# Kernel optimization log

Measured on AMD Instinct MI355X. Metric: run time of the kernel, lower is better.

The kernel has to match this reference:

```python
import jax, jax.numpy as jnp
import numpy as np

EPS = 1e-6
B, S, H, I = 4, 2048, 2048, 8192  # batch, seq, hidden(embed), intermediate(mlp)
N_ACT = 2  # gated: ('gelu', 'linear')


def setup_inputs() -> dict:
    key = jax.random.key(0)
    k_x, k_k1, k_k2 = jax.random.split(key, 3)
    x = jax.random.normal(k_x, (B, S, H), dtype=jnp.float32)
    scale = jnp.ones((H,), dtype=jnp.float32)          # layernorm gamma (ones init)
    ln_bias = jnp.zeros((H,), dtype=jnp.float32)       # layernorm beta (zeros init)
    # kernel_1: (hidden, n_activations, intermediate); kernel_2: (intermediate, hidden)
    kernel_1 = jax.random.normal(k_k1, (H, N_ACT, I), dtype=jnp.float32) * 0.02
    kernel_2 = jax.random.normal(k_k2, (I, H), dtype=jnp.float32) * 0.02
    return {"x": x, "scale": scale, "ln_bias": ln_bias, "kernel_1": kernel_1, "kernel_2": kernel_2}


def reference(x, scale, ln_bias, kernel_1, kernel_2):
    # LayerNorm over last axis (zero_centered_gamma=False)
    mean = jnp.mean(x, axis=-1, keepdims=True)
    var = jnp.mean(jnp.square(x - mean), axis=-1, keepdims=True)
    ln = (x - mean) * jax.lax.rsqrt(var + EPS) * scale + ln_bias  # [B,S,H]
    # Dense 1: project to (n_activations, intermediate)
    y = jnp.einsum('bsh,hai->bsai', ln, kernel_1)  # [B,S,2,I]
    # Gated activation: gelu(y0) * linear(y1)  (flax nn.gelu default approximate=True)
    z = jax.nn.gelu(y[..., 0, :], approximate=True) * y[..., 1, :]  # [B,S,I]
    # Dense 2: project back to hidden
    out = jnp.einsum('bsi,ih->bsh', z, kernel_2)  # [B,S,H]
    return out
```

## Files before the change

### kernel.cpp

```cpp
#include <hip/hip_runtime.h>
#include <hip/hip_bf16.h>

#define DEVINL __device__ __forceinline__

typedef __attribute__((ext_vector_type(8))) __bf16 bf16x8;
typedef __attribute__((ext_vector_type(4))) float f32x4;
typedef __attribute__((ext_vector_type(4))) unsigned short us4;

DEVINL unsigned short f2bf(float f) {
  union { float f; unsigned int u; } c;
  c.f = f;
  unsigned int u = c.u;
  u += 0x7fffu + ((u >> 16) & 1u);
  return (unsigned short)(u >> 16);
}

DEVINL float gelu_tanh(float x) {
  float t = 1.5957691216057308f * x * __builtin_fmaf(0.044715f, x * x, 1.0f);
  return x / (1.0f + __expf(-t));
}

DEVINL void ld16(const void* g, void* l) {
  __builtin_amdgcn_global_load_lds(
      (const __attribute__((address_space(1))) void*)g,
      (__attribute__((address_space(3))) void*)l, 16, 0, 0);
}

__global__ __launch_bounds__(256) void transpose_cast_kernel(
    const float* __restrict__ in, unsigned short* __restrict__ out, int R, int C) {
  __shared__ float tile[32][33];
  const int t = threadIdx.x;
  const int r0 = blockIdx.x << 5, c0 = blockIdx.y << 5;
  const int tr = t >> 3, tc = (t & 7) << 2;
  const float4 v = *(const float4*)(in + (size_t)(r0 + tr) * C + c0 + tc);
  tile[tr][tc] = v.x; tile[tr][tc + 1] = v.y;
  tile[tr][tc + 2] = v.z; tile[tr][tc + 3] = v.w;
  __syncthreads();
  us4 o;
  o[0] = f2bf(tile[tc + 0][tr]);
  o[1] = f2bf(tile[tc + 1][tr]);
  o[2] = f2bf(tile[tc + 2][tr]);
  o[3] = f2bf(tile[tc + 3][tr]);
  *(us4*)(out + (size_t)(c0 + tr) * R + r0 + tc) = o;
}

__global__ __launch_bounds__(256) void ln_kernel(
    const float* __restrict__ x, const float* __restrict__ gamma,
    const float* __restrict__ beta, unsigned short* __restrict__ out) {
  constexpr int H = 2048;
  const int t = threadIdx.x;
  const size_t row = blockIdx.x;
  const float4* xr = (const float4*)(x + row * H);
  const float4 a = xr[t], b = xr[t + 256];
  float s  = a.x + a.y + a.z + a.w + b.x + b.y + b.z + b.w;
  float s2 = a.x*a.x + a.y*a.y + a.z*a.z + a.w*a.w
           + b.x*b.x + b.y*b.y + b.z*b.z + b.w*b.w;
#pragma unroll
  for (int o = 32; o > 0; o >>= 1) { s += __shfl_xor(s, o); s2 += __shfl_xor(s2, o); }
  __shared__ float red[8];
  const int wid = t >> 6, lane = t & 63;
  if (lane == 0) { red[wid] = s; red[4 + wid] = s2; }
  __syncthreads();
  s  = red[0] + red[1] + red[2] + red[3];
  s2 = red[4] + red[5] + red[6] + red[7];
  const float mean = s * (1.0f / H);
  const float rstd = rsqrtf(s2 * (1.0f / H) - mean * mean + 1e-6f);
  const float4 g0 = ((const float4*)gamma)[t], g1 = ((const float4*)gamma)[t + 256];
  const float4 c0 = ((const float4*)beta)[t],  c1 = ((const float4*)beta)[t + 256];
  us4 o0, o1;
  o0[0] = f2bf((a.x - mean) * rstd * g0.x + c0.x);
  o0[1] = f2bf((a.y - mean) * rstd * g0.y + c0.y);
  o0[2] = f2bf((a.z - mean) * rstd * g0.z + c0.z);
  o0[3] = f2bf((a.w - mean) * rstd * g0.w + c0.w);
  o1[0] = f2bf((b.x - mean) * rstd * g1.x + c1.x);
  o1[1] = f2bf((b.y - mean) * rstd * g1.y + c1.y);
  o1[2] = f2bf((b.z - mean) * rstd * g1.z + c1.z);
  o1[3] = f2bf((b.w - mean) * rstd * g1.w + c1.w);
  *(us4*)(out + row * H + (size_t)t * 4) = o0;
  *(us4*)(out + row * H + 1024 + (size_t)t * 4) = o1;
}

template<int KDIM, bool GATED>
__global__ __launch_bounds__(512, 2) void gemm8p(
    const unsigned short* __restrict__ Amat,
    const unsigned short* __restrict__ Bm0,
    const unsigned short* __restrict__ Bm1,
    void* __restrict__ outp, int mCount) {
  constexpr int NT = KDIM / 64;
  __shared__ char lds[131072];
  const int t = threadIdx.x, lane = t & 63, wid = t >> 6;
  const int wr = wid >> 2, wc = wid & 3;
  const int bid = (int)blockIdx.x;
  int mb, nb;
  if (GATED && mCount >= 8) {
    const int xcd = bid & 7, l = bid >> 3;
    const int g = l >> 5, l32 = l & 31;
    const int mchunks = mCount >> 3;
    const int quad = g / mchunks, mch = g % mchunks;
    mb = (mch << 3) | (l32 & 7);
    nb = (xcd << 3) | (quad << 2) | (l32 >> 3);
  } else {
    const int nwg = (int)gridDim.x, q = nwg >> 3;
    const int wg = (bid & 7) * q + (bid >> 3);
    mb = wg % mCount; nb = wg / mCount;
  }
  const size_t m0 = (size_t)mb << 8;
  const size_t nrow = (size_t)nb * (GATED ? 128 : 256);
  const unsigned short* aSrc  = Amat + m0 * KDIM;
  const unsigned short* b0Src = Bm0 + nrow * KDIM;
  const unsigned short* b1Src = Bm1 + nrow * KDIM;

  const int srow = (wid << 3) + (lane >> 3);
  const int sOff = srow * KDIM + (((lane & 7) ^ (srow & 7)) << 3);

  const int fr = lane & 15, l16 = lane >> 4;
  const int c0 = (l16 ^ (fr & 7)) << 4;
  const int c1 = ((4 | l16) ^ (fr & 7)) << 4;
  const int aRowOff = ((wr << 6) + fr) << 7;
  const int bRowOff = ((wc << 5) + fr) << 7;

  f32x4 acc[2][2][4][2] = {};

  auto stageU = [&](const unsigned short* src, int ldsOff, int k0) {
    const unsigned short* s = src + sOff + k0;
    ld16(s, lds + ldsOff + (wid << 10));
    ld16(s + (size_t)64 * KDIM, lds + ldsOff + 8192 + (wid << 10));
  };

#define READ_A(dst_, ab_)                                                     \
  _Pragma("unroll") for (int m = 0; m < 4; ++m) {                             \
    dst_[0][m] = *(const bf16x8*)((ab_) + aRowOff + m * 2048 + c0);           \
    dst_[1][m] = *(const bf16x8*)((ab_) + aRowOff + m * 2048 + c1);           \
  }
#define READ_B(dst_, bb_)                                                     \
  _Pragma("unroll") for (int n = 0; n < 2; ++n) {                             \
    dst_[0][n] = *(const bf16x8*)((bb_) + bRowOff + n * 2048 + c0);           \
    dst_[1][n] = *(const bf16x8*)((bb_) + bRowOff + n * 2048 + c1);           \
  }
#define MFMA16(mh_, g_, bsrc_)                                                \
  __builtin_amdgcn_s_setprio(1);                                              \
  _Pragma("unroll") for (int m = 0; m < 4; ++m)                               \
    _Pragma("unroll") for (int n = 0; n < 2; ++n) {                           \
      acc[mh_][g_][m][n] = __builtin_amdgcn_mfma_f32_16x16x32_bf16(           \
          af[0][m], bsrc_[0][n], acc[mh_][g_][m][n], 0, 0, 0);                \
      acc[mh_][g_][m][n] = __builtin_amdgcn_mfma_f32_16x16x32_bf16(           \
          af[1][m], bsrc_[1][n], acc[mh_][g_][m][n], 0, 0, 0);                \
    }                                                                         \
  __builtin_amdgcn_s_setprio(0);
#define LGKM(n_)                                                              \
  asm volatile("s_waitcnt lgkmcnt(" #n_ ")" ::: "memory");                    \
  __builtin_amdgcn_sched_barrier(0);

  stageU(aSrc, 0, 0);
  stageU(b0Src, 32768, 0);
  stageU(aSrc + (size_t)128 * KDIM, 16384, 0);
  stageU(b1Src, 49152, 0);
  stageU(aSrc, 65536, 64);
  stageU(b0Src, 65536 + 32768, 64);
  asm volatile("s_waitcnt vmcnt(4)" ::: "memory");
  __builtin_amdgcn_s_barrier();

  for (int tt = 0; tt < NT; ++tt) {
    const int c = tt & 1, cn = c ^ 1;
    const int t1 = (tt + 1 < NT) ? tt + 1 : NT - 1;
    const int t2 = (tt + 2 < NT) ? tt + 2 : NT - 1;
    const int k1b = t1 << 6, k2b = t2 << 6;
    const int cb = c << 16, cnb = cn << 16;
    const char* base = lds + cb;
    bf16x8 af[2][4], b0r[2][2], b1r[2][2];

    READ_A(af, base);
    READ_B(b0r, base + 32768);
    READ_B(b1r, base + 49152);
    stageU(aSrc + (size_t)128 * KDIM, cnb + 16384, k1b);
    LGKM(4);
    MFMA16(0, 0, b0r);
    LGKM(0);
    MFMA16(0, 1, b1r);
    READ_A(af, base + 16384);
    stageU(b1Src, cnb + 49152, k1b);
    __builtin_amdgcn_s_barrier();
    LGKM(0);
    MFMA16(1, 1, b1r);
    MFMA16(1, 0, b0r);
    stageU(aSrc, cb, k2b);
    stageU(b0Src, cb + 32768, k2b);
    asm volatile("s_waitcnt vmcnt(4)" ::: "memory");
    __builtin_amdgcn_s_barrier();
  }
  asm volatile("s_waitcnt vmcnt(0)" ::: "memory");
#undef READ_A
#undef READ_B
#undef MFMA16
#undef LGKM

  const int fq = (lane >> 4) << 2;
  if constexpr (GATED) {
    unsigned short* Z = (unsigned short*)outp;
#pragma unroll
    for (int mh = 0; mh < 2; ++mh)
#pragma unroll
      for (int m = 0; m < 4; ++m)
#pragma unroll
        for (int n = 0; n < 2; ++n) {
          const size_t row = m0 + (mh << 7) + (wr << 6) + (m << 4) + fq;
          const size_t col = ((size_t)nb << 7) + (wc << 5) + (n << 4) + fr;
#pragma unroll
          for (int rr = 0; rr < 4; ++rr) {
            const float y0 = acc[mh][0][m][n][rr];
            const float y1 = acc[mh][1][m][n][rr];
            Z[(row + rr) * 8192 + col] = f2bf(gelu_tanh(y0) * y1);
          }
        }
  } else {
    float* O = (float*)outp;
#pragma unroll
    for (int mh = 0; mh < 2; ++mh)
#pragma unroll
      for (int g = 0; g < 2; ++g)
#pragma unroll
        for (int m = 0; m < 4; ++m)
#pragma unroll
          for (int n = 0; n < 2; ++n) {
            const size_t row = m0 + (mh << 7) + (wr << 6) + (m << 4) + fq;
            const size_t col = ((size_t)nb << 8) + (g << 7) + (wc << 5) + (n << 4) + fr;
#pragma unroll
            for (int rr = 0; rr < 4; ++rr)
              O[(row + rr) * 2048 + col] = acc[mh][g][m][n][rr];
          }
  }
}

extern "C" void kernel_launch(void* const* d_in, const int* in_sizes, int n_in,
                              void* d_out, int out_size, void* d_ws, size_t ws_size,
                              hipStream_t stream) {
  const float* x     = (const float*)d_in[0];
  const float* gamma = (const float*)d_in[1];
  const float* beta  = (const float*)d_in[2];
  const float* k1    = (const float*)d_in[3];
  const float* k2    = (const float*)d_in[4];
  float* out = (float*)d_out;

  const size_t H = 2048, I = 8192, M = 8192;
  unsigned short* k1T = (unsigned short*)d_ws;
  unsigned short* k2T = k1T + 2 * I * H;
  unsigned short* lnb = k2T + H * I;
  unsigned short* zb  = lnb + M * H;

  const size_t fixedB = (2 * I * H + H * I + M * H) * 2;
  int nc = 1;
  while (nc < 32 && fixedB + (M / nc) * I * 2 > ws_size) nc <<= 1;

  transpose_cast_kernel<<<dim3(H / 32, (2 * I) / 32), 256, 0, stream>>>(
      k1, k1T, (int)H, (int)(2 * I));
  transpose_cast_kernel<<<dim3(I / 32, H / 32), 256, 0, stream>>>(
      k2, k2T, (int)I, (int)H);
  ln_kernel<<<dim3((unsigned)M), 256, 0, stream>>>(x, gamma, beta, lnb);

  const size_t Mc = M / nc;
  const int mC = (int)(Mc / 256);
  for (int c = 0; c < nc; ++c) {
    gemm8p<2048, true><<<dim3((unsigned)(mC * 64)), 512, 0, stream>>>(
        lnb + c * Mc * H, k1T, k1T + (size_t)8192 * 2048, zb, mC);
    gemm8p<8192, false><<<dim3((unsigned)(mC * 8)), 512, 0, stream>>>(
        zb, k2T, k2T + (size_t)128 * 8192, out + c * Mc * H, mC);
  }
}
```

Measured before the change: 770.5 us.

## Software-pipeline LDS fragment reads across K tiles with double register sets

Restructures the GEMM main loop so the next tile's LDS fragment reads are issued before the second half of the current tile's MFMAs, using two alternating register sets (X/Y) and a loop unrolled by two. Global staging loads are also moved earlier in each tile. The aim is to hide LDS read latency behind MFMA work instead of stalling at the start of each iteration. In exchange it raises register pressure, which could lower occupancy or cause spills, and it assumes NT is even.

```diff
diff --git a/kernel.cpp b/kernel.cpp
--- a/kernel.cpp
+++ b/kernel.cpp
@@ -137,19 +137,20 @@
     dst_[0][n] = *(const bf16x8*)((bb_) + bRowOff + n * 2048 + c0);           \
     dst_[1][n] = *(const bf16x8*)((bb_) + bRowOff + n * 2048 + c1);           \
   }
-#define MFMA16(mh_, g_, bsrc_)                                                \
+#define MFMA16(mh_, g_, afr_, bsrc_)                                          \
   __builtin_amdgcn_s_setprio(1);                                              \
   _Pragma("unroll") for (int m = 0; m < 4; ++m)                               \
     _Pragma("unroll") for (int n = 0; n < 2; ++n) {                           \
       acc[mh_][g_][m][n] = __builtin_amdgcn_mfma_f32_16x16x32_bf16(           \
-          af[0][m], bsrc_[0][n], acc[mh_][g_][m][n], 0, 0, 0);                \
+          afr_[0][m], bsrc_[0][n], acc[mh_][g_][m][n], 0, 0, 0);              \
       acc[mh_][g_][m][n] = __builtin_amdgcn_mfma_f32_16x16x32_bf16(           \
-          af[1][m], bsrc_[1][n], acc[mh_][g_][m][n], 0, 0, 0);                \
+          afr_[1][m], bsrc_[1][n], acc[mh_][g_][m][n], 0, 0, 0);              \
     }                                                                         \
   __builtin_amdgcn_s_setprio(0);
 #define LGKM(n_)                                                              \
   asm volatile("s_waitcnt lgkmcnt(" #n_ ")" ::: "memory");                    \
   __builtin_amdgcn_sched_barrier(0);
+#define SCHED0 __builtin_amdgcn_sched_barrier(0)
 
   stageU(aSrc, 0, 0);
   stageU(b0Src, 32768, 0);
@@ -160,39 +161,53 @@
   asm volatile("s_waitcnt vmcnt(4)" ::: "memory");
   __builtin_amdgcn_s_barrier();
 
-  for (int tt = 0; tt < NT; ++tt) {
-    const int c = tt & 1, cn = c ^ 1;
-    const int t1 = (tt + 1 < NT) ? tt + 1 : NT - 1;
-    const int t2 = (tt + 2 < NT) ? tt + 2 : NT - 1;
-    const int k1b = t1 << 6, k2b = t2 << 6;
-    const int cb = c << 16, cnb = cn << 16;
-    const char* base = lds + cb;
-    bf16x8 af[2][4], b0r[2][2], b1r[2][2];
-
-    READ_A(af, base);
-    READ_B(b0r, base + 32768);
-    READ_B(b1r, base + 49152);
-    stageU(aSrc + (size_t)128 * KDIM, cnb + 16384, k1b);
-    LGKM(4);
-    MFMA16(0, 0, b0r);
-    LGKM(0);
-    MFMA16(0, 1, b1r);
-    READ_A(af, base + 16384);
-    stageU(b1Src, cnb + 49152, k1b);
-    __builtin_amdgcn_s_barrier();
-    LGKM(0);
-    MFMA16(1, 1, b1r);
-    MFMA16(1, 0, b0r);
-    stageU(aSrc, cb, k2b);
-    stageU(b0Src, cb + 32768, k2b);
-    asm volatile("s_waitcnt vmcnt(4)" ::: "memory");
-    __builtin_amdgcn_s_barrier();
-  }
-  asm volatile("s_waitcnt vmcnt(0)" ::: "memory");
+  bf16x8 afX[2][4], b0X[2][2], b1X[2][2];
+  bf16x8 afY[2][4], b0Y[2][2], b1Y[2][2];
+  READ_A(afX, lds);          SCHED0;
+  READ_B(b0X, lds + 32768);  SCHED0;
+  READ_B(b1X, lds + 49152);  SCHED0;
+
+#define TILE(tt_, cb_, cnb_, AF, B0R, B1R, AFN, B0N, B1N)                      \
+  {                                                                            \
+    const int t1 = ((tt_) + 1 < NT) ? (tt_) + 1 : NT - 1;                      \
+    const int t2 = ((tt_) + 2 < NT) ? (tt_) + 2 : NT - 1;                      \
+    const int k1b = t1 << 6, k2b = t2 << 6;                                    \
+    const char* base = lds + (cb_);                                            \
+    const char* nbase = lds + (cnb_);                                          \
+                                                                       \
+    LGKM(4);                                            \
+    stageU(aSrc + (size_t)128 * KDIM, (cnb_) + 16384, k1b);     \
+    stageU(b1Src, (cnb_) + 49152, k1b);                         \
+    MFMA16(0, 0, AF, B0R);                                                     \
+    LGKM(0);                                                    \
+    MFMA16(0, 1, AF, B1R);                                                     \
+    READ_A(AF, base + 16384); SCHED0;               \
+    __builtin_amdgcn_s_barrier();                                   \
+    LGKM(0);                                                  \
+                                                                       \
+    stageU(aSrc, (cb_), k2b);                                   \
+    stageU(b0Src, (cb_) + 32768, k2b);                          \
+    asm volatile("s_waitcnt vmcnt(4)" ::: "memory");     \
+    SCHED0;                                                                    \
+    __builtin_amdgcn_s_barrier();                                   \
+    READ_A(AFN, nbase);           SCHED0;           \
+    READ_B(B0N, nbase + 32768);   SCHED0;                                      \
+    READ_B(B1N, nbase + 49152);   SCHED0;                                      \
+    MFMA16(1, 1, AF, B1R);                        \
+    MFMA16(1, 0, AF, B0R);                                                     \
+  }
+
+  for (int tt = 0; tt < NT; tt += 2) {
+    TILE(tt,     0,     65536, afX, b0X, b1X, afY, b0Y, b1Y);
+    TILE(tt + 1, 65536, 0,     afY, b0Y, b1Y, afX, b0X, b1X);
+  }
+  asm volatile("s_waitcnt vmcnt(0) lgkmcnt(0)" ::: "memory");
+#undef TILE
 #undef READ_A
 #undef READ_B
 #undef MFMA16
 #undef LGKM
+#undef SCHED0
 
   const int fq = (lane >> 4) << 2;
   if constexpr (GATED) {
```

After: 2.567 ms. +233.1%, slower.

## Load B operand directly from global into registers, deepen A LDS ring to four slots

Applied to the files above, without the earlier changes.

The B (weight) operand is no longer staged through LDS; each wave loads its B fragments straight from global memory into double-buffered registers one tile ahead. LDS now holds only the A tile, arranged as a four-slot ring with a two-tile prefetch distance, and the main loop is unrolled by four to rotate slots and register buffers. The aim is to cut LDS traffic and ds_read work for B and spend LDS on deeper A prefetch. In exchange, B global loads are not shared across the waves that need the same columns, which raises global/L2 traffic and register pressure, and latency hiding now depends on the vmcnt waits.

```diff
diff --git a/kernel.cpp b/kernel.cpp
--- a/kernel.cpp
+++ b/kernel.cpp
@@ -81,7 +81,7 @@
 }
 
 template<int KDIM, bool GATED>
-__global__ __launch_bounds__(512, 2) void gemm8p(
+__global__ __launch_bounds__(512, 2) void gemm_bd(
     const unsigned short* __restrict__ Amat,
     const unsigned short* __restrict__ Bm0,
     const unsigned short* __restrict__ Bm1,
@@ -117,82 +117,89 @@
   const int c0 = (l16 ^ (fr & 7)) << 4;
   const int c1 = ((4 | l16) ^ (fr & 7)) << 4;
   const int aRowOff = ((wr << 6) + fr) << 7;
-  const int bRowOff = ((wc << 5) + fr) << 7;
+
+  const size_t bOff = (size_t)((wc << 5) + fr) * KDIM + (size_t)(l16 << 3);
 
   f32x4 acc[2][2][4][2] = {};
 
-  auto stageU = [&](const unsigned short* src, int ldsOff, int k0) {
-    const unsigned short* s = src + sOff + k0;
-    ld16(s, lds + ldsOff + (wid << 10));
-    ld16(s + (size_t)64 * KDIM, lds + ldsOff + 8192 + (wid << 10));
+  auto stageA = [&](int slotBase, int k0) {
+    const unsigned short* s = aSrc + sOff + k0;
+    char* d = lds + slotBase + (wid << 10);
+    ld16(s, d);
+    ld16(s + (size_t)64 * KDIM, d + 8192);
+    ld16(s + (size_t)128 * KDIM, d + 16384);
+    ld16(s + (size_t)192 * KDIM, d + 24576);
   };
 
-#define READ_A(dst_, ab_)                                                     \
+#define READ_A(ab_)                                                           \
   _Pragma("unroll") for (int m = 0; m < 4; ++m) {                             \
-    dst_[0][m] = *(const bf16x8*)((ab_) + aRowOff + m * 2048 + c0);           \
-    dst_[1][m] = *(const bf16x8*)((ab_) + aRowOff + m * 2048 + c1);           \
-  }
-#define READ_B(dst_, bb_)                                                     \
+    af[0][m] = *(const bf16x8*)((ab_) + aRowOff + m * 2048 + c0);             \
+    af[1][m] = *(const bf16x8*)((ab_) + aRowOff + m * 2048 + c1);             \
+  }
+#define LOAD_B(d0_, d1_, k0_)                                                 \
   _Pragma("unroll") for (int n = 0; n < 2; ++n) {                             \
-    dst_[0][n] = *(const bf16x8*)((bb_) + bRowOff + n * 2048 + c0);           \
-    dst_[1][n] = *(const bf16x8*)((bb_) + bRowOff + n * 2048 + c1);           \
+    const unsigned short* p0 = b0Src + bOff + (size_t)(n * 16) * KDIM + (k0_);\
+    const unsigned short* p1 = b1Src + bOff + (size_t)(n * 16) * KDIM + (k0_);\
+    d0_[0][n] = *(const bf16x8*)(p0);                                         \
+    d0_[1][n] = *(const bf16x8*)(p0 + 32);                                    \
+    d1_[0][n] = *(const bf16x8*)(p1);                                         \
+    d1_[1][n] = *(const bf16x8*)(p1 + 32);                                    \
   }
 #define MFMA16(mh_, g_, bsrc_)                                                \
-  __builtin_amdgcn_s_setprio(1);                                              \
   _Pragma("unroll") for (int m = 0; m < 4; ++m)                               \
     _Pragma("unroll") for (int n = 0; n < 2; ++n) {                           \
       acc[mh_][g_][m][n] = __builtin_amdgcn_mfma_f32_16x16x32_bf16(           \
           af[0][m], bsrc_[0][n], acc[mh_][g_][m][n], 0, 0, 0);                \
       acc[mh_][g_][m][n] = __builtin_amdgcn_mfma_f32_16x16x32_bf16(           \
           af[1][m], bsrc_[1][n], acc[mh_][g_][m][n], 0, 0, 0);                \
-    }                                                                         \
-  __builtin_amdgcn_s_setprio(0);
-#define LGKM(n_)                                                              \
-  asm volatile("s_waitcnt lgkmcnt(" #n_ ")" ::: "memory");                    \
-  __builtin_amdgcn_sched_barrier(0);
-
-  stageU(aSrc, 0, 0);
-  stageU(b0Src, 32768, 0);
-  stageU(aSrc + (size_t)128 * KDIM, 16384, 0);
-  stageU(b1Src, 49152, 0);
-  stageU(aSrc, 65536, 64);
-  stageU(b0Src, 65536 + 32768, 64);
-  asm volatile("s_waitcnt vmcnt(4)" ::: "memory");
+    }
+#define SCHED0 __builtin_amdgcn_sched_barrier(0)
+
+  bf16x8 af[2][4];
+  bf16x8 b0X[2][2], b1X[2][2], b0Y[2][2], b1Y[2][2];
+
+  stageA(0, 0);
+  LOAD_B(b0X, b1X, 0);
+  stageA(32768, NT > 1 ? 64 : 0);
+  asm volatile("s_waitcnt vmcnt(12)" ::: "memory");
   __builtin_amdgcn_s_barrier();
 
-  for (int tt = 0; tt < NT; ++tt) {
-    const int c = tt & 1, cn = c ^ 1;
-    const int t1 = (tt + 1 < NT) ? tt + 1 : NT - 1;
-    const int t2 = (tt + 2 < NT) ? tt + 2 : NT - 1;
-    const int k1b = t1 << 6, k2b = t2 << 6;
-    const int cb = c << 16, cnb = cn << 16;
-    const char* base = lds + cb;
-    bf16x8 af[2][4], b0r[2][2], b1r[2][2];
-
-    READ_A(af, base);
-    READ_B(b0r, base + 32768);
-    READ_B(b1r, base + 49152);
-    stageU(aSrc + (size_t)128 * KDIM, cnb + 16384, k1b);
-    LGKM(4);
-    MFMA16(0, 0, b0r);
-    LGKM(0);
-    MFMA16(0, 1, b1r);
-    READ_A(af, base + 16384);
-    stageU(b1Src, cnb + 49152, k1b);
-    __builtin_amdgcn_s_barrier();
-    LGKM(0);
-    MFMA16(1, 1, b1r);
-    MFMA16(1, 0, b0r);
-    stageU(aSrc, cb, k2b);
-    stageU(b0Src, cb + 32768, k2b);
-    asm volatile("s_waitcnt vmcnt(4)" ::: "memory");
-    __builtin_amdgcn_s_barrier();
-  }
-  asm volatile("s_waitcnt vmcnt(0)" ::: "memory");
+#define TILE(tt_, SL_, SL2_, BC0, BC1, BN0, BN1)                               \
+  {                                                                            \
+    const int t1 = ((tt_) + 1 < NT) ? (tt_) + 1 : NT - 1;                      \
+    const int t2 = ((tt_) + 2 < NT) ? (tt_) + 2 : NT - 1;                      \
+    LOAD_B(BN0, BN1, t1 << 6);                                                 \
+    READ_A(lds + (SL_) * 32768);                                 \
+    SCHED0;                                                                    \
+    __builtin_amdgcn_s_setprio(1);                                             \
+    MFMA16(0, 0, BC0);                                                         \
+    MFMA16(0, 1, BC1);                                                         \
+    __builtin_amdgcn_s_setprio(0);                                             \
+    SCHED0;                                                                    \
+    READ_A(lds + (SL_) * 32768 + 16384);      \
+    stageA((SL2_) * 32768, t2 << 6);                  \
+    SCHED0;                                                                    \
+    __builtin_amdgcn_s_setprio(1);                                             \
+    MFMA16(1, 1, BC1);                                                         \
+    MFMA16(1, 0, BC0);                                                         \
+    __builtin_amdgcn_s_setprio(0);                                             \
+    SCHED0;                                                                    \
+    asm volatile("s_waitcnt vmcnt(12)" ::: "memory");     \
+    __builtin_amdgcn_s_barrier();             \
+  }
+
+  for (int tt = 0; tt < NT; tt += 4) {
+    TILE(tt,     0, 2, b0X, b1X, b0Y, b1Y);
+    TILE(tt + 1, 1, 3, b0Y, b1Y, b0X, b1X);
+    TILE(tt + 2, 2, 0, b0X, b1X, b0Y, b1Y);
+    TILE(tt + 3, 3, 1, b0Y, b1Y, b0X, b1X);
+  }
+  asm volatile("s_waitcnt vmcnt(0) lgkmcnt(0)" ::: "memory");
+#undef TILE
 #undef READ_A
-#undef READ_B
+#undef LOAD_B
 #undef MFMA16
-#undef LGKM
+#undef SCHED0
 
   const int fq = (lane >> 4) << 2;
   if constexpr (GATED) {
@@ -260,9 +267,9 @@
   const size_t Mc = M / nc;
   const int mC = (int)(Mc / 256);
   for (int c = 0; c < nc; ++c) {
-    gemm8p<2048, true><<<dim3((unsigned)(mC * 64)), 512, 0, stream>>>(
+    gemm_bd<2048, true><<<dim3((unsigned)(mC * 64)), 512, 0, stream>>>(
         lnb + c * Mc * H, k1T, k1T + (size_t)8192 * 2048, zb, mC);
-    gemm8p<8192, false><<<dim3((unsigned)(mC * 8)), 512, 0, stream>>>(
+    gemm_bd<8192, false><<<dim3((unsigned)(mC * 8)), 512, 0, stream>>>(
         zb, k2T, k2T + (size_t)128 * 8192, out + c * Mc * H, mC);
   }
 }
```

After: 1.104 ms. 43.3% more time.
